# Optimization experiments

Measured on AMD Instinct MI355X. Metric: run time of the kernel, lower is better.

## Reference

```python
import jax, jax.numpy as jnp
import numpy as np

N_NODES = 100000
N_EDGES = 1600000
IN_FEATS = 128
OUT_FEATS = 48


def setup_inputs() -> dict:
    key = jax.random.key(0)
    ks = jax.random.split(key, 6)
    features = jax.random.normal(ks[0], (N_NODES, IN_FEATS), dtype=jnp.float32)
    # xavier_uniform for W.weight [out, in]
    lim_w = float(np.sqrt(6.0 / (IN_FEATS + OUT_FEATS)))
    W_w = jax.random.uniform(ks[1], (OUT_FEATS, IN_FEATS), dtype=jnp.float32, minval=-lim_w, maxval=lim_w)
    W_b = jnp.zeros((OUT_FEATS,), dtype=jnp.float32)
    # xavier_uniform for attn_w [2*out, 1]
    lim_a = float(np.sqrt(6.0 / (2 * OUT_FEATS + 1)))
    attn_w = jax.random.uniform(ks[2], (2 * OUT_FEATS, 1), dtype=jnp.float32, minval=-lim_a, maxval=lim_a)
    attn_b = jnp.zeros((1,), dtype=jnp.float32)
    src = jax.random.randint(ks[3], (N_EDGES,), 0, N_NODES, dtype=jnp.int32)
    dst = jax.random.randint(ks[4], (N_EDGES,), 0, N_NODES, dtype=jnp.int32)
    return {"features": features, "W_w": W_w, "W_b": W_b,
            "attn_w": attn_w, "attn_b": attn_b, "src": src, "dst": dst}


def reference(features, W_w, W_b, attn_w, attn_b, src, dst):
    n = features.shape[0]
    d = W_w.shape[0]
    # h = W(features)  [N, d]
    h = features @ W_w.T + W_b
    # cat([h[src], h[dst]]) @ attn_w == h[src] @ w_src + h[dst] @ w_dst
    w_src = attn_w[:d, 0]   # [d]
    w_dst = attn_w[d:, 0]   # [d]
    s_src = h @ w_src       # [N]
    s_dst = h @ w_dst       # [N]
    e = s_src[src] + s_dst[dst] + attn_b[0]            # [E]
    e = jax.nn.leaky_relu(e, negative_slope=0.2)
    # edge softmax grouped by destination node
    m = jax.ops.segment_max(e, dst, num_segments=n)     # [N]
    ex = jnp.exp(e - m[dst])                            # [E]
    denom = jax.ops.segment_sum(ex, dst, num_segments=n)  # [N]
    alpha = ex / denom[dst]                             # [E]
    # weighted scatter-sum: out[v] = sum_{(u,v) in E} alpha * h[u]
    msgs = h[src] * alpha[:, None]                      # [E, d]
    out = jax.ops.segment_sum(msgs, dst, num_segments=n)  # [N, d]
    return out
```

## Files before the change

### kernel.cpp

```cpp
#include <hip/hip_runtime.h>

#define NFEAT 128
#define DOUT 48
#define BSH 6
#define BNODES 64
#define PCAP 192
#define BCAP (PCAP * 8)
#define EPT 16
#define NBMAX 1568
#define HSTRIDE 32

typedef __attribute__((ext_vector_type(8))) short bf16x8;
typedef __attribute__((ext_vector_type(4))) float f32x4;

__device__ __forceinline__ float bf_lo(unsigned u) { return __uint_as_float(u << 16); }
__device__ __forceinline__ float bf_hi(unsigned u) { return __uint_as_float(u & 0xFFFF0000u); }
__device__ __forceinline__ unsigned bf_pack(float a, float b) {
    unsigned ua = __float_as_uint(a), ub = __float_as_uint(b);
    ua = (ua + 0x7FFFu + ((ua >> 16) & 1u)) >> 16;
    ub = (ub + 0x7FFFu + ((ub >> 16) & 1u)) & 0xFFFF0000u;
    return ua | ub;
}

__device__ __forceinline__ void split2(float x, short& hi, short& lo) {
    unsigned u = __float_as_uint(x);
    unsigned h = u & 0xFFFF0000u;
    hi = (short)(h >> 16);
    float r = x - __uint_as_float(h);
    unsigned v = __float_as_uint(r);
    lo = (short)((v + 0x7FFFu + ((v >> 16) & 1u)) >> 16);
}

__global__ __launch_bounds__(256) void k_proj(
    const float* __restrict__ feat, const float* __restrict__ Ww,
    const float* __restrict__ Wb, const float* __restrict__ attn_w,
    unsigned* __restrict__ hbf, float* __restrict__ s_src, float* __restrict__ s_dst,
    int n)
{
    __shared__ float hb[128][49];

    int tid  = threadIdx.x;
    int lane = tid & 63;
    int wv   = tid >> 6;
    int g    = lane >> 4;
    int r16  = lane & 15;

    int mbase = blockIdx.x * 128 + wv * 32;
    int na0 = mbase + r16;       if (na0 >= n) na0 = n - 1;
    int na1 = mbase + 16 + r16;  if (na1 >= n) na1 = n - 1;

    const float* fA0 = feat + (size_t)na0 * NFEAT + g * 4;
    const float* fA1 = feat + (size_t)na1 * NFEAT + g * 4;
    const float* wB  = Ww + (size_t)r16 * NFEAT + g * 4;

    f32x4 acc[2][3];
#pragma unroll
    for (int mt = 0; mt < 2; ++mt)
#pragma unroll
        for (int nt = 0; nt < 3; ++nt)
            acc[mt][nt] = (f32x4){0.f, 0.f, 0.f, 0.f};

#pragma unroll
    for (int ks = 0; ks < 4; ++ks) {
        f32x4 ra[4], rb[6];
        ra[0] = *(const f32x4*)(fA0 + ks * 32);
        ra[1] = *(const f32x4*)(fA0 + ks * 32 + 16);
        ra[2] = *(const f32x4*)(fA1 + ks * 32);
        ra[3] = *(const f32x4*)(fA1 + ks * 32 + 16);
        rb[0] = *(const f32x4*)(wB + ks * 32);
        rb[1] = *(const f32x4*)(wB + ks * 32 + 16);
        rb[2] = *(const f32x4*)(wB + 16 * NFEAT + ks * 32);
        rb[3] = *(const f32x4*)(wB + 16 * NFEAT + ks * 32 + 16);
        rb[4] = *(const f32x4*)(wB + 32 * NFEAT + ks * 32);
        rb[5] = *(const f32x4*)(wB + 32 * NFEAT + ks * 32 + 16);

        bf16x8 Ah[2], Al[2], Bh[3], Bl[3];
#pragma unroll
        for (int t = 0; t < 2; ++t) {
#pragma unroll
            for (int i = 0; i < 4; ++i) {
                short h, l;
                split2(ra[2 * t][i], h, l);     Ah[t][i] = h;     Al[t][i] = l;
                split2(ra[2 * t + 1][i], h, l); Ah[t][i + 4] = h; Al[t][i + 4] = l;
            }
        }
#pragma unroll
        for (int t = 0; t < 3; ++t) {
#pragma unroll
            for (int i = 0; i < 4; ++i) {
                short h, l;
                split2(rb[2 * t][i], h, l);     Bh[t][i] = h;     Bl[t][i] = l;
                split2(rb[2 * t + 1][i], h, l); Bh[t][i + 4] = h; Bl[t][i + 4] = l;
            }
        }
#pragma unroll
        for (int mt = 0; mt < 2; ++mt)
#pragma unroll
            for (int nt = 0; nt < 3; ++nt) {
                acc[mt][nt] = __builtin_amdgcn_mfma_f32_16x16x32_bf16(Ah[mt], Bh[nt], acc[mt][nt], 0, 0, 0);
                acc[mt][nt] = __builtin_amdgcn_mfma_f32_16x16x32_bf16(Al[mt], Bh[nt], acc[mt][nt], 0, 0, 0);
                acc[mt][nt] = __builtin_amdgcn_mfma_f32_16x16x32_bf16(Ah[mt], Bl[nt], acc[mt][nt], 0, 0, 0);
            }
    }

#pragma unroll
    for (int mt = 0; mt < 2; ++mt)
#pragma unroll
        for (int nt = 0; nt < 3; ++nt)
#pragma unroll
            for (int rr = 0; rr < 4; ++rr)
                hb[wv * 32 + mt * 16 + 4 * g + rr][nt * 16 + r16] = acc[mt][nt][rr];
    __syncthreads();

    int node = tid >> 1, part = tid & 1, jb = part * 24;
    int gn = blockIdx.x * 128 + node;
    float v[24];
    float ss = 0.f, sd = 0.f;
#pragma unroll
    for (int j = 0; j < 24; ++j) {
        float x = hb[node][jb + j] + Wb[jb + j];
        v[j] = x;
        ss = fmaf(x, attn_w[jb + j], ss);
        sd = fmaf(x, attn_w[DOUT + jb + j], sd);
    }
    ss += __shfl_xor(ss, 1, 64);
    sd += __shfl_xor(sd, 1, 64);

    if (gn < n) {
        uint4* hp = (uint4*)(hbf + (size_t)gn * HSTRIDE + part * 12);
#pragma unroll
        for (int q = 0; q < 3; ++q) {
            uint4 u;
            u.x = bf_pack(v[8 * q + 0], v[8 * q + 1]);
            u.y = bf_pack(v[8 * q + 2], v[8 * q + 3]);
            u.z = bf_pack(v[8 * q + 4], v[8 * q + 5]);
            u.w = bf_pack(v[8 * q + 6], v[8 * q + 7]);
            hp[q] = u;
        }
        if (part == 0) {
            s_src[gn] = ss;
            s_dst[gn] = sd;
        }
    }
}

__global__ __launch_bounds__(256) void k_bin(
    const int4* __restrict__ src4, const int4* __restrict__ dst4,
    const float* __restrict__ s_src, const float* __restrict__ s_dst,
    const float* __restrict__ attn_b,
    int* __restrict__ cursor, int2* __restrict__ ents, int nE, int NB)
{
    __shared__ int hist[NBMAX];
    __shared__ int bas[NBMAX];

    int tid = threadIdx.x;
    int cls = blockIdx.x & 7;
    long long e0 = (long long)blockIdx.x * 4096 + (long long)tid * EPT;

    for (int t = tid; t < NB; t += 256) hist[t] = 0;
    __syncthreads();

    int s[EPT], d[EPT];
    bool any = (e0 < nE);
#pragma unroll
    for (int q = 0; q < EPT / 4; ++q) {
        int4 sv = any ? src4[e0 / 4 + q] : make_int4(0, 0, 0, 0);
        int4 dv = any ? dst4[e0 / 4 + q] : make_int4(0, 0, 0, 0);
        s[4 * q + 0] = sv.x; s[4 * q + 1] = sv.y; s[4 * q + 2] = sv.z; s[4 * q + 3] = sv.w;
        d[4 * q + 0] = dv.x; d[4 * q + 1] = dv.y; d[4 * q + 2] = dv.z; d[4 * q + 3] = dv.w;
    }

    float vs[EPT], vd[EPT];
#pragma unroll
    for (int u = 0; u < EPT; ++u) vs[u] = s_src[s[u]];
#pragma unroll
    for (int u = 0; u < EPT; ++u) vd[u] = s_dst[d[u]];

    int rank[EPT];
#pragma unroll
    for (int u = 0; u < EPT; ++u)
        rank[u] = (e0 + u < nE) ? atomicAdd(&hist[d[u] >> BSH], 1) : 0;
    __syncthreads();

    for (int t = tid; t < NB; t += 256) {
        int c = hist[t];
        if (c > 0) bas[t] = atomicAdd(cursor + cls * NB + t, c);
    }
    __syncthreads();

    float ab = attn_b[0];
#pragma unroll
    for (int u = 0; u < EPT; ++u) {
        if (e0 + u < nE) {
            float v = vs[u] + vd[u] + ab;
            v = (v > 0.f) ? v : 0.2f * v;
            float x = __expf(v);
            int bkt = d[u] >> BSH;
            int slot = bas[bkt] + rank[u];
            if (slot < PCAP)
                ents[(size_t)bkt * BCAP + cls * PCAP + slot] =
                    make_int2(s[u] | ((d[u] & (BNODES - 1)) << 17), __float_as_int(x));
        }
    }
}

__global__ __launch_bounds__(512) void k_aggb(
    const unsigned* __restrict__ hbf, const int* __restrict__ cursor,
    const int2* __restrict__ ents, float* __restrict__ out, int n, int NB)
{
    __shared__ int2 se[BCAP];
    __shared__ int2 sse[BCAP];
    __shared__ int c1[BNODES], c2[BNODES], lrp[BNODES + 1];
    __shared__ int cp[9];

    int b = blockIdx.x;
    int tid = threadIdx.x;

    if (tid < BNODES) { c1[tid] = 0; c2[tid] = 0; }
    if (tid < 8) {
        int c = min(cursor[tid * NB + b], PCAP);
        int p = c;
#pragma unroll
        for (int o = 1; o < 8; o <<= 1) {
            int u = __shfl_up(p, o, 64);
            if (tid >= o) p += u;
        }
        cp[tid + 1] = p;
        if (tid == 0) cp[0] = 0;
    }
    __syncthreads();
    int total = cp[8];

    for (int i = tid; i < total; i += 512) {
        int c = 0;
        while (i >= cp[c + 1]) ++c;
        int2 v = ents[(size_t)b * BCAP + c * PCAP + (i - cp[c])];
        se[i] = v;
        atomicAdd(&c1[((unsigned)v.x) >> 17], 1);
    }
    __syncthreads();

    if (tid < BNODES) {
        int v = c1[tid];
        int p = v;
#pragma unroll
        for (int o = 1; o < 64; o <<= 1) {
            int u = __shfl_up(p, o, 64);
            if (tid >= o) p += u;
        }
        lrp[tid] = p - v;
        if (tid == BNODES - 1) lrp[BNODES] = p;
    }
    __syncthreads();

    for (int i = tid; i < total; i += 512) {
        int2 v = se[i];
        int dl = ((unsigned)v.x) >> 17;
        int pos = lrp[dl] + atomicAdd(&c2[dl], 1);
        sse[pos] = v;
    }
    __syncthreads();

    int wave = tid >> 6, lane = tid & 63;
    int g = lane >> 3, sub = lane & 7;
    for (int dl = wave; dl < BNODES; dl += 8) {
        int node = (b << BSH) + dl;
        if (node >= n) break;
        int st = lrp[dl], en = lrp[dl + 1];
        float a0 = 0.f, a1 = 0.f, a2 = 0.f, a3 = 0.f, a4 = 0.f, a5 = 0.f, den = 0.f;
        int k = st + g;
        for (; k + 8 < en; k += 16) {
            int2 e1 = sse[k];
            int2 e2 = sse[k + 8];
            const unsigned* h1 = hbf + (size_t)(e1.x & 0x1FFFF) * HSTRIDE + sub * 3;
            const unsigned* h2 = hbf + (size_t)(e2.x & 0x1FFFF) * HSTRIDE + sub * 3;
            unsigned u10 = h1[0], u11 = h1[1], u12 = h1[2];
            unsigned u20 = h2[0], u21 = h2[1], u22 = h2[2];
            float x1 = __int_as_float(e1.y), x2 = __int_as_float(e2.y);
            den += x1; den += x2;
            a0 = fmaf(x1, bf_lo(u10), a0);
            a1 = fmaf(x1, bf_hi(u10), a1);
            a2 = fmaf(x1, bf_lo(u11), a2);
            a3 = fmaf(x1, bf_hi(u11), a3);
            a4 = fmaf(x1, bf_lo(u12), a4);
            a5 = fmaf(x1, bf_hi(u12), a5);
            a0 = fmaf(x2, bf_lo(u20), a0);
            a1 = fmaf(x2, bf_hi(u20), a1);
            a2 = fmaf(x2, bf_lo(u21), a2);
            a3 = fmaf(x2, bf_hi(u21), a3);
            a4 = fmaf(x2, bf_lo(u22), a4);
            a5 = fmaf(x2, bf_hi(u22), a5);
        }
        if (k < en) {
            int2 ed = sse[k];
            float x = __int_as_float(ed.y);
            den += x;
            const unsigned* hr = hbf + (size_t)(ed.x & 0x1FFFF) * HSTRIDE + sub * 3;
            unsigned u0 = hr[0], u1 = hr[1], u2 = hr[2];
            a0 = fmaf(x, bf_lo(u0), a0);
            a1 = fmaf(x, bf_hi(u0), a1);
            a2 = fmaf(x, bf_lo(u1), a2);
            a3 = fmaf(x, bf_hi(u1), a3);
            a4 = fmaf(x, bf_lo(u2), a4);
            a5 = fmaf(x, bf_hi(u2), a5);
        }
#pragma unroll
        for (int o = 8; o <= 32; o <<= 1) {
            a0  += __shfl_xor(a0, o, 64);
            a1  += __shfl_xor(a1, o, 64);
            a2  += __shfl_xor(a2, o, 64);
            a3  += __shfl_xor(a3, o, 64);
            a4  += __shfl_xor(a4, o, 64);
            a5  += __shfl_xor(a5, o, 64);
            den += __shfl_xor(den, o, 64);
        }
        if (lane < 8) {
            float inv = (en > st) ? 1.f / den : 0.f;
            float* op = out + (size_t)node * DOUT + sub * 6;
            op[0] = a0 * inv;
            op[1] = a1 * inv;
            op[2] = a2 * inv;
            op[3] = a3 * inv;
            op[4] = a4 * inv;
            op[5] = a5 * inv;
        }
    }
}

extern "C" void kernel_launch(void* const* d_in, const int* in_sizes, int n_in,
                              void* d_out, int out_size, void* d_ws, size_t ws_size,
                              hipStream_t stream) {
    const float* feat   = (const float*)d_in[0];
    const float* Ww     = (const float*)d_in[1];
    const float* Wb     = (const float*)d_in[2];
    const float* attn_w = (const float*)d_in[3];
    const float* attn_b = (const float*)d_in[4];
    const int*   src    = (const int*)d_in[5];
    const int*   dst    = (const int*)d_in[6];

    int n  = in_sizes[0] / NFEAT;
    int nE = in_sizes[5];
    int NB = (n + BNODES - 1) / BNODES;
    int N8 = NB * 8;
    float* out = (float*)d_out;

    unsigned* hbf  = (unsigned*)d_ws;
    float* s_src   = (float*)(hbf + (size_t)n * HSTRIDE);
    float* s_dst   = s_src + n;
    int*   cursor  = (int*)(s_dst + n);
    int2*  ents    = (int2*)(cursor + N8);

    hipMemsetAsync(cursor, 0, (size_t)N8 * sizeof(int), stream);

    int NBp = (n + 127) / 128;
    k_proj<<<NBp, 256, 0, stream>>>(feat, Ww, Wb, attn_w, hbf, s_src, s_dst, n);
    int nbb = (nE + 4095) / 4096;
    k_bin<<<nbb, 256, 0, stream>>>((const int4*)src, (const int4*)dst,
                                   s_src, s_dst, attn_b, cursor, ents, nE, NB);
    k_aggb<<<NB, 512, 0, stream>>>(hbf, cursor, ents, out, n, NB);
}
```

Before: 187.3 us.

## Pad bf16 feature rows to 16-byte chunks and shrink aggregation block

Each node's bf16 row is re-laid out as eight 16-byte chunks of six values plus padding, so each aggregation lane gathers its slice with a single 128-bit load instead of three scalar loads. The aggregation kernel drops the first shared staging buffer and reads entries from global memory twice, once for counting and once for scattering. It also runs 256 threads per block instead of 512, which halves shared memory per block and may raise occupancy. The cost is wasted bandwidth on the padded lanes and a second global read of the edge entries.

```diff
diff --git a/kernel.cpp b/kernel.cpp
--- a/kernel.cpp
+++ b/kernel.cpp
@@ -127,15 +127,15 @@
     sd += __shfl_xor(sd, 1, 64);
 
     if (gn < n) {
-        uint4* hp = (uint4*)(hbf + (size_t)gn * HSTRIDE + part * 12);
-#pragma unroll
-        for (int q = 0; q < 3; ++q) {
+#pragma unroll
+        for (int q = 0; q < 4; ++q) {
+            int sub = part * 4 + q;
             uint4 u;
-            u.x = bf_pack(v[8 * q + 0], v[8 * q + 1]);
-            u.y = bf_pack(v[8 * q + 2], v[8 * q + 3]);
-            u.z = bf_pack(v[8 * q + 4], v[8 * q + 5]);
-            u.w = bf_pack(v[8 * q + 6], v[8 * q + 7]);
-            hp[q] = u;
+            u.x = bf_pack(v[6 * q + 0], v[6 * q + 1]);
+            u.y = bf_pack(v[6 * q + 2], v[6 * q + 3]);
+            u.z = bf_pack(v[6 * q + 4], v[6 * q + 5]);
+            u.w = 0;
+            *(uint4*)(hbf + (size_t)gn * HSTRIDE + sub * 4) = u;
         }
         if (part == 0) {
             s_src[gn] = ss;
@@ -204,17 +204,17 @@
     }
 }
 
-__global__ __launch_bounds__(512) void k_aggb(
+__global__ __launch_bounds__(256) void k_aggb(
     const unsigned* __restrict__ hbf, const int* __restrict__ cursor,
     const int2* __restrict__ ents, float* __restrict__ out, int n, int NB)
 {
-    __shared__ int2 se[BCAP];
     __shared__ int2 sse[BCAP];
     __shared__ int c1[BNODES], c2[BNODES], lrp[BNODES + 1];
     __shared__ int cp[9];
 
     int b = blockIdx.x;
     int tid = threadIdx.x;
+    const int2* ebase = ents + (size_t)b * BCAP;
 
     if (tid < BNODES) { c1[tid] = 0; c2[tid] = 0; }
     if (tid < 8) {
@@ -231,12 +231,11 @@
     __syncthreads();
     int total = cp[8];
 
-    for (int i = tid; i < total; i += 512) {
+    for (int i = tid; i < total; i += 256) {
         int c = 0;
         while (i >= cp[c + 1]) ++c;
-        int2 v = ents[(size_t)b * BCAP + c * PCAP + (i - cp[c])];
-        se[i] = v;
-        atomicAdd(&c1[((unsigned)v.x) >> 17], 1);
+        int x = ebase[c * PCAP + (i - cp[c])].x;
+        atomicAdd(&c1[((unsigned)x) >> 17], 1);
     }
     __syncthreads();
 
@@ -253,8 +252,10 @@
     }
     __syncthreads();
 
-    for (int i = tid; i < total; i += 512) {
-        int2 v = se[i];
+    for (int i = tid; i < total; i += 256) {
+        int c = 0;
+        while (i >= cp[c + 1]) ++c;
+        int2 v = ebase[c * PCAP + (i - cp[c])];
         int dl = ((unsigned)v.x) >> 17;
         int pos = lrp[dl] + atomicAdd(&c2[dl], 1);
         sse[pos] = v;
@@ -263,7 +264,7 @@
 
     int wave = tid >> 6, lane = tid & 63;
     int g = lane >> 3, sub = lane & 7;
-    for (int dl = wave; dl < BNODES; dl += 8) {
+    for (int dl = wave; dl < BNODES; dl += 4) {
         int node = (b << BSH) + dl;
         if (node >= n) break;
         int st = lrp[dl], en = lrp[dl + 1];
@@ -272,37 +273,34 @@
         for (; k + 8 < en; k += 16) {
             int2 e1 = sse[k];
             int2 e2 = sse[k + 8];
-            const unsigned* h1 = hbf + (size_t)(e1.x & 0x1FFFF) * HSTRIDE + sub * 3;
-            const unsigned* h2 = hbf + (size_t)(e2.x & 0x1FFFF) * HSTRIDE + sub * 3;
-            unsigned u10 = h1[0], u11 = h1[1], u12 = h1[2];
-            unsigned u20 = h2[0], u21 = h2[1], u22 = h2[2];
+            uint4 h1 = *(const uint4*)(hbf + (size_t)(e1.x & 0x1FFFF) * HSTRIDE + sub * 4);
+            uint4 h2 = *(const uint4*)(hbf + (size_t)(e2.x & 0x1FFFF) * HSTRIDE + sub * 4);
             float x1 = __int_as_float(e1.y), x2 = __int_as_float(e2.y);
             den += x1; den += x2;
-            a0 = fmaf(x1, bf_lo(u10), a0);
-            a1 = fmaf(x1, bf_hi(u10), a1);
-            a2 = fmaf(x1, bf_lo(u11), a2);
-            a3 = fmaf(x1, bf_hi(u11), a3);
-            a4 = fmaf(x1, bf_lo(u12), a4);
-            a5 = fmaf(x1, bf_hi(u12), a5);
-            a0 = fmaf(x2, bf_lo(u20), a0);
-            a1 = fmaf(x2, bf_hi(u20), a1);
-            a2 = fmaf(x2, bf_lo(u21), a2);
-            a3 = fmaf(x2, bf_hi(u21), a3);
-            a4 = fmaf(x2, bf_lo(u22), a4);
-            a5 = fmaf(x2, bf_hi(u22), a5);
+            a0 = fmaf(x1, bf_lo(h1.x), a0);
+            a1 = fmaf(x1, bf_hi(h1.x), a1);
+            a2 = fmaf(x1, bf_lo(h1.y), a2);
+            a3 = fmaf(x1, bf_hi(h1.y), a3);
+            a4 = fmaf(x1, bf_lo(h1.z), a4);
+            a5 = fmaf(x1, bf_hi(h1.z), a5);
+            a0 = fmaf(x2, bf_lo(h2.x), a0);
+            a1 = fmaf(x2, bf_hi(h2.x), a1);
+            a2 = fmaf(x2, bf_lo(h2.y), a2);
+            a3 = fmaf(x2, bf_hi(h2.y), a3);
+            a4 = fmaf(x2, bf_lo(h2.z), a4);
+            a5 = fmaf(x2, bf_hi(h2.z), a5);
         }
         if (k < en) {
             int2 ed = sse[k];
             float x = __int_as_float(ed.y);
             den += x;
-            const unsigned* hr = hbf + (size_t)(ed.x & 0x1FFFF) * HSTRIDE + sub * 3;
-            unsigned u0 = hr[0], u1 = hr[1], u2 = hr[2];
-            a0 = fmaf(x, bf_lo(u0), a0);
-            a1 = fmaf(x, bf_hi(u0), a1);
-            a2 = fmaf(x, bf_lo(u1), a2);
-            a3 = fmaf(x, bf_hi(u1), a3);
-            a4 = fmaf(x, bf_lo(u2), a4);
-            a5 = fmaf(x, bf_hi(u2), a5);
+            uint4 h0 = *(const uint4*)(hbf + (size_t)(ed.x & 0x1FFFF) * HSTRIDE + sub * 4);
+            a0 = fmaf(x, bf_lo(h0.x), a0);
+            a1 = fmaf(x, bf_hi(h0.x), a1);
+            a2 = fmaf(x, bf_lo(h0.y), a2);
+            a3 = fmaf(x, bf_hi(h0.y), a3);
+            a4 = fmaf(x, bf_lo(h0.z), a4);
+            a5 = fmaf(x, bf_hi(h0.z), a5);
         }
 #pragma unroll
         for (int o = 8; o <= 32; o <<= 1) {
@@ -357,5 +355,5 @@
     int nbb = (nE + 4095) / 4096;
     k_bin<<<nbb, 256, 0, stream>>>((const int4*)src, (const int4*)dst,
                                    s_src, s_dst, attn_b, cursor, ents, nE, NB);
-    k_aggb<<<NB, 512, 0, stream>>>(hbf, cursor, ents, out, n, NB);
-}
+    k_aggb<<<NB, 256, 0, stream>>>(hbf, cursor, ents, out, n, NB);
+}
```

After: 190.4 us. Within noise of the previous version (+1.7%).
